# Performance work log

Measured on AMD Instinct MI355X. Metric: run time of the kernel, lower is better.

The kernel has to match this reference:

```python
import jax, jax.numpy as jnp
import numpy as np

NEG_SLOPE = 0.2   # PyG GATConv default negative_slope
BN_EPS = 1e-5


def gat_layer(x, src, dst, W, a_src, a_dst, b, num_nodes):
    """PyG-style GATConv (concat=True). src/dst already include self-loops."""
    H, C = a_src.shape
    h = (x @ W).reshape(num_nodes, H, C)            # [N,H,C]
    al_s = jnp.sum(h * a_src, axis=-1)              # [N,H] per-node src score
    al_d = jnp.sum(h * a_dst, axis=-1)              # [N,H]
    e = al_s[src] + al_d[dst]                       # [E,H]
    e = jnp.where(e > 0, e, NEG_SLOPE * e)          # leaky_relu
    m = jax.ops.segment_max(e, dst, num_segments=num_nodes)
    e = jnp.exp(e - m[dst])
    s = jax.ops.segment_sum(e, dst, num_segments=num_nodes)
    alpha = e / (s[dst] + 1e-16)                    # segment softmax over dst
    out = jax.ops.segment_sum(alpha[:, :, None] * h[src], dst, num_segments=num_nodes)
    return out.reshape(num_nodes, H * C) + b


def batch_norm(x, gamma, beta):
    mu = jnp.mean(x, axis=0)
    var = jnp.mean((x - mu) ** 2, axis=0)
    return (x - mu) * jax.lax.rsqrt(var + BN_EPS) * gamma + beta


def setup_inputs() -> dict:
    N, E, IN, H, C, L, OUT, NC = 50000, 800000, 256, 4, 64, 32, 32, 30
    HC = H * C
    key = jax.random.key(0)
    cnt = [0]
    def nk():
        cnt[0] += 1
        return jax.random.fold_in(key, cnt[0])
    def w(shape, scale):
        return jax.random.normal(nk(), shape, jnp.float32) * scale
    inp = {
        "x": jax.random.normal(nk(), (N, IN), jnp.float32),
        "edge_index": jax.random.randint(nk(), (2, E), 0, N, dtype=jnp.int32),
        "eps": jax.random.normal(nk(), (N, L), jnp.float32),
    }
    for i, d_in in zip((1, 2, 3), (IN, HC, HC)):
        inp[f"W{i}"] = w((d_in, HC), 1.0 / np.sqrt(d_in))
        inp[f"asrc{i}"] = w((H, C), 0.1)
        inp[f"adst{i}"] = w((H, C), 0.1)
        inp[f"b{i}"] = jnp.zeros((HC,), jnp.float32)
        inp[f"g{i}"] = jnp.ones((HC,), jnp.float32)
        inp[f"be{i}"] = jnp.zeros((HC,), jnp.float32)
    inp["Wr"] = w((IN, HC), 1.0 / np.sqrt(IN)); inp["br"] = jnp.zeros((HC,), jnp.float32)
    inp["Wmu"] = w((HC, L), 1.0 / np.sqrt(HC)); inp["bmu"] = jnp.zeros((L,), jnp.float32)
    inp["Wlv"] = w((HC, L), 1.0 / np.sqrt(HC)); inp["blv"] = jnp.zeros((L,), jnp.float32)
    inp["Wd"] = w((L, OUT), 1.0 / np.sqrt(L)); inp["bd"] = jnp.zeros((OUT,), jnp.float32)
    inp["Wa"] = w((HC, NC), 1.0 / np.sqrt(HC)); inp["ba"] = jnp.zeros((NC,), jnp.float32)
    return inp


def reference(x, edge_index, eps,
              W1, asrc1, adst1, b1, g1, be1,
              W2, asrc2, adst2, b2, g2, be2,
              W3, asrc3, adst3, b3, g3, be3,
              Wr, br, Wmu, bmu, Wlv, blv, Wd, bd, Wa, ba):
    N = x.shape[0]
    loop = jnp.arange(N, dtype=edge_index.dtype)   # PyG add_self_loops default
    src = jnp.concatenate([edge_index[0], loop])
    dst = jnp.concatenate([edge_index[1], loop])

    residual = x @ Wr + br                          # [N, HC]
    h = jax.nn.relu(batch_norm(gat_layer(x, src, dst, W1, asrc1, adst1, b1, N), g1, be1))
    h = jax.nn.relu(batch_norm(gat_layer(h, src, dst, W2, asrc2, adst2, b2, N), g2, be2))
    h = jax.nn.relu(batch_norm(gat_layer(h, src, dst, W3, asrc3, adst3, b3, N), g3, be3))
    enc = h + residual

    mu = enc @ Wmu + bmu
    logvar = enc @ Wlv + blv
    z = mu + eps * jnp.exp(0.5 * logvar)            # reparameterize
    out = z @ Wd + bd
    aux_out = enc @ Wa + ba
    return (out, mu, logvar, aux_out, enc)
```

## Files before the change

### kernel.cpp

```cpp
#include <hip/hip_runtime.h>
#include <cstdint>

typedef __bf16 bf16;
typedef float f32x4 __attribute__((ext_vector_type(4)));
typedef _Float16 fp16;
typedef _Float16 half8 __attribute__((ext_vector_type(8)));

#define NEG_SLOPE 0.2f
#define BN_EPS 1e-5f

__device__ __forceinline__ void gld_lds16(const void* g, void* l) {
  auto gp = reinterpret_cast<const __attribute__((address_space(1))) unsigned int*>(
      reinterpret_cast<uintptr_t>(g));
  auto lp = reinterpret_cast<__attribute__((address_space(3))) unsigned int*>(
      reinterpret_cast<uintptr_t>(l));
  __builtin_amdgcn_global_load_lds(gp, lp, 16, 0, 0);
}

__global__ void k_init_counts(int* counts, int N) {
  int i = blockIdx.x * 256 + threadIdx.x;
  if (i < N) counts[i] = 1;
}

__global__ void k_count(const int* __restrict__ ei, int* counts, int E) {
  int i = blockIdx.x * 256 + threadIdx.x;
  if (i < E) atomicAdd(&counts[ei[E + i]], 1);
}

__global__ __launch_bounds__(256) void k_scan1(const int* __restrict__ counts,
                                               int* __restrict__ row_start,
                                               int* __restrict__ bsums, int N) {
  __shared__ int s[256];
  const int t = threadIdx.x;
  const int idx = blockIdx.x * 1024 + t * 4;
  int a0 = (idx + 0 < N) ? counts[idx + 0] : 0;
  int a1 = (idx + 1 < N) ? counts[idx + 1] : 0;
  int a2 = (idx + 2 < N) ? counts[idx + 2] : 0;
  int a3 = (idx + 3 < N) ? counts[idx + 3] : 0;
  const int mysum = a0 + a1 + a2 + a3;
  s[t] = mysum;
  __syncthreads();
  for (int ofs = 1; ofs < 256; ofs <<= 1) {
    int v = (t >= ofs) ? s[t - ofs] : 0;
    __syncthreads();
    s[t] += v;
    __syncthreads();
  }
  int excl = s[t] - mysum;
  if (idx + 0 < N) row_start[idx + 0] = excl;
  if (idx + 1 < N) row_start[idx + 1] = excl + a0;
  if (idx + 2 < N) row_start[idx + 2] = excl + a0 + a1;
  if (idx + 3 < N) row_start[idx + 3] = excl + a0 + a1 + a2;
  if (t == 255) bsums[blockIdx.x] = s[255];
}

__global__ void k_scan2(int* __restrict__ bsums, int* __restrict__ row_start, int nb, int N) {
  if (threadIdx.x == 0 && blockIdx.x == 0) {
    int run = 0;
    for (int i = 0; i < nb; ++i) {
      int v = bsums[i];
      bsums[i] = run;
      run += v;
    }
    row_start[N] = run;
  }
}

__global__ void k_scan3(int* __restrict__ row_start, int* __restrict__ cursor,
                        const int* __restrict__ bsums, int N) {
  int i = blockIdx.x * 256 + threadIdx.x;
  if (i < N) {
    int v = row_start[i] + bsums[i >> 10];
    row_start[i] = v;
    cursor[i] = v;
  }
}

__global__ void k_fill(const int* __restrict__ ei, int* cursor, int* __restrict__ csr_src,
                       int E, int N) {
  int i = blockIdx.x * 256 + threadIdx.x;
  if (i < E) {
    int s = ei[i], d = ei[E + i];
    int p = atomicAdd(&cursor[d], 1);
    csr_src[p] = s;
  } else if (i < E + N) {
    int n = i - E;
    int p = atomicAdd(&cursor[n], 1);
    csr_src[p] = n;
  }
}

__global__ void k_tofp16(const float* __restrict__ src, fp16* __restrict__ dst, int n) {
  int i = blockIdx.x * 256 + threadIdx.x;
  if (i < n) dst[i] = (fp16)src[i];
}

__global__ void k_transpose_w(const float* __restrict__ W, fp16* __restrict__ Wt) {
  int k = blockIdx.x, n = threadIdx.x;
  Wt[n * 256 + k] = (fp16)W[k * 256 + n];
}

__global__ void k_build_head_w(const float* __restrict__ Wmu, const float* __restrict__ bmu,
                               const float* __restrict__ Wlv, const float* __restrict__ blv,
                               const float* __restrict__ Wa, const float* __restrict__ ba,
                               fp16* __restrict__ Wh, float* __restrict__ bias_cat) {
  int k = blockIdx.x, n = threadIdx.x;
  float v = 0.f;
  if (n < 32) v = Wmu[k * 32 + n];
  else if (n < 64) v = Wlv[k * 32 + (n - 32)];
  else if (n < 94) v = Wa[k * 30 + (n - 64)];
  Wh[n * 256 + k] = (fp16)v;
  if (k == 0) {
    float b = 0.f;
    if (n < 32) b = bmu[n];
    else if (n < 64) b = blv[n - 32];
    else if (n < 94) b = ba[n - 64];
    bias_cat[n] = b;
  }
}

__global__ __launch_bounds__(256) void k_gemm(
    const fp16* __restrict__ A16, const fp16* __restrict__ B16,
    const float* __restrict__ bias, float* __restrict__ Cf, fp16* __restrict__ C16,
    const float* __restrict__ asrcp, const float* __restrict__ adstp,
    float* __restrict__ alsp, float* __restrict__ aldp,
    int M, int ldc) {
  __shared__ fp16 Ash[128 * 32];
  __shared__ fp16 Bsh[128 * 32];
  const int t = threadIdx.x;
  const int wave = t >> 6, lane = t & 63;
  const int m0 = blockIdx.x * 128, n0 = blockIdx.y * 128;
  const int lrow = lane & 15, lq = lane >> 4;
  const int wm = (wave >> 1) * 64, wn = (wave & 1) * 64;

  f32x4 acc[4][4] = {};

  const int j0 = wave * 64 + lane, j1 = j0 + 256;
  const int ar0 = j0 >> 2, ar1 = j1 >> 2;
  const int ak0 = ((j0 & 3) ^ ((ar0 >> 1) & 3)) * 8;
  const int ak1 = ((j1 & 3) ^ ((ar1 >> 1) & 3)) * 8;
  const int gm0 = min(m0 + ar0, M - 1), gm1 = min(m0 + ar1, M - 1);
  const size_t oa0 = (size_t)gm0 * 256 + ak0, oa1 = (size_t)gm1 * 256 + ak1;
  const size_t ob0 = (size_t)(n0 + ar0) * 256 + ak0, ob1 = (size_t)(n0 + ar1) * 256 + ak1;
  const int l0 = wave * 512, l1 = 2048 + wave * 512;

  for (int k0 = 0; k0 < 256; k0 += 32) {
    __syncthreads();
    gld_lds16(A16 + oa0 + k0, Ash + l0);
    gld_lds16(A16 + oa1 + k0, Ash + l1);
    gld_lds16(B16 + ob0 + k0, Bsh + l0);
    gld_lds16(B16 + ob1 + k0, Bsh + l1);
    __syncthreads();
    half8 af[4], bf[4];
#pragma unroll
    for (int mi = 0; mi < 4; mi++) {
      int row = wm + mi * 16 + lrow;
      int off = row * 32 + ((lq ^ ((row >> 1) & 3)) << 3);
      af[mi] = *(const half8*)(Ash + off);
    }
#pragma unroll
    for (int ni = 0; ni < 4; ni++) {
      int row = wn + ni * 16 + lrow;
      int off = row * 32 + ((lq ^ ((row >> 1) & 3)) << 3);
      bf[ni] = *(const half8*)(Bsh + off);
    }
#pragma unroll
    for (int mi = 0; mi < 4; mi++)
#pragma unroll
      for (int ni = 0; ni < 4; ni++)
        acc[mi][ni] = __builtin_amdgcn_mfma_f32_16x16x32_f16(af[mi], bf[ni], acc[mi][ni], 0, 0, 0);
  }

#pragma unroll
  for (int mi = 0; mi < 4; mi++) {
    const int mb = m0 + wm + mi * 16 + lq * 4;
#pragma unroll
    for (int ni = 0; ni < 4; ni++) {
      const int n = n0 + wn + ni * 16 + lrow;
#pragma unroll
      for (int r = 0; r < 4; r++) {
        int m = mb + r;
        if (m < M) {
          if (C16) C16[(size_t)m * ldc + n] = (fp16)acc[mi][ni][r];
          else     Cf[(size_t)m * ldc + n] = acc[mi][ni][r] + (bias ? bias[n] : 0.f);
        }
      }
    }
  }

  if (asrcp) {
    const int headg = (n0 + wn) >> 6;
    float as4[4], ad4[4];
#pragma unroll
    for (int ni = 0; ni < 4; ni++) {
      int cg = n0 + wn + ni * 16 + lrow;
      as4[ni] = asrcp[cg];
      ad4[ni] = adstp[cg];
    }
#pragma unroll
    for (int mi = 0; mi < 4; mi++) {
      float ps[4] = {0.f, 0.f, 0.f, 0.f}, pd[4] = {0.f, 0.f, 0.f, 0.f};
#pragma unroll
      for (int ni = 0; ni < 4; ni++)
#pragma unroll
        for (int r = 0; r < 4; r++) {
          ps[r] += acc[mi][ni][r] * as4[ni];
          pd[r] += acc[mi][ni][r] * ad4[ni];
        }
#pragma unroll
      for (int o = 1; o < 16; o <<= 1)
#pragma unroll
        for (int r = 0; r < 4; r++) {
          ps[r] += __shfl_xor(ps[r], o, 64);
          pd[r] += __shfl_xor(pd[r], o, 64);
        }
      if (lrow == 0) {
#pragma unroll
        for (int r = 0; r < 4; r++) {
          int m = m0 + wm + mi * 16 + lq * 4 + r;
          if (m < M) {
            alsp[(size_t)m * 4 + headg] = ps[r];
            aldp[(size_t)m * 4 + headg] = pd[r];
          }
        }
      }
    }
  }
}

__global__ __launch_bounds__(256) void k_gather(
    const fp16* __restrict__ h16, const float* __restrict__ als, const float* __restrict__ ald,
    const int* __restrict__ row_start, const int* __restrict__ csr_src,
    const float* __restrict__ bias, fp16* __restrict__ out, float* __restrict__ stats, int N) {
  if (blockIdx.x == 0) { stats[threadIdx.x] = 0.f; stats[256 + threadIdx.x] = 0.f; }
  const int wave = threadIdx.x >> 6, lane = threadIdx.x & 63;
  const int half = lane >> 5, l32 = lane & 31;
  const int n = blockIdx.x * 8 + wave * 2 + half;
  if (n >= N) return;
  const int head = l32 >> 3;
  const int c0 = l32 * 8;
  const float adh = ald[(size_t)n * 4 + head];
  const int beg = row_start[n], end = row_start[n + 1];
  float s = 0.f;
  float acc[8] = {0.f, 0.f, 0.f, 0.f, 0.f, 0.f, 0.f, 0.f};
#pragma unroll 4
  for (int i = beg; i < end; ++i) {
    const int sidx = csr_src[i];
    float e = als[(size_t)sidx * 4 + head] + adh;
    e = e > 0.f ? e : NEG_SLOPE * e;
    const float w = __expf(e);
    s += w;
    const half8 hv = *(const half8*)(h16 + (size_t)sidx * 256 + c0);
#pragma unroll
    for (int k = 0; k < 8; ++k) acc[k] += w * (float)hv[k];
  }
  const float inv = 1.f / (s + 1e-16f);
  const float4 b1 = *(const float4*)(bias + c0);
  const float4 b2 = *(const float4*)(bias + c0 + 4);
  half8 o;
  o[0] = (fp16)(acc[0] * inv + b1.x); o[1] = (fp16)(acc[1] * inv + b1.y);
  o[2] = (fp16)(acc[2] * inv + b1.z); o[3] = (fp16)(acc[3] * inv + b1.w);
  o[4] = (fp16)(acc[4] * inv + b2.x); o[5] = (fp16)(acc[5] * inv + b2.y);
  o[6] = (fp16)(acc[6] * inv + b2.z); o[7] = (fp16)(acc[7] * inv + b2.w);
  *(half8*)(out + (size_t)n * 256 + c0) = o;
}

__global__ __launch_bounds__(256) void k_bn_stats(const fp16* __restrict__ x,
                                                  float* __restrict__ stats, int N) {
  const int t = threadIdx.x;
  int r0 = blockIdx.x * 128;
  int rend = min(r0 + 128, N);
  float s = 0.f, sq = 0.f;
  for (int r = r0; r < rend; ++r) {
    float v = (float)x[(size_t)r * 256 + t];
    s += v; sq += v * v;
  }
  atomicAdd(&stats[t], s);
  atomicAdd(&stats[256 + t], sq);
}

__global__ __launch_bounds__(256) void k_bn_apply(
    const fp16* __restrict__ x, const float* __restrict__ stats,
    const float* __restrict__ g, const float* __restrict__ be,
    fp16* __restrict__ act16, float* __restrict__ encf,
    float invN, int total) {
  int idx = blockIdx.x * 256 + threadIdx.x;
  if (idx >= total) return;
  int c = idx & 255;
  float mu = stats[c] * invN;
  float var = stats[256 + c] * invN - mu * mu;
  float v = ((float)x[idx] - mu) * rsqrtf(var + BN_EPS) * g[c] + be[c];
  v = fmaxf(v, 0.f);
  if (encf) { v += encf[idx]; encf[idx] = v; }
  act16[idx] = (fp16)v;
}

__global__ __launch_bounds__(256) void k_finish(
    const float* __restrict__ HEAD, const float* __restrict__ eps,
    const float* __restrict__ Wd, const float* __restrict__ bd,
    float* __restrict__ o_out, float* __restrict__ o_mu, float* __restrict__ o_lv,
    float* __restrict__ o_aux, int N) {
  __shared__ float sWd[1024];
  __shared__ float sZ[8][33];
  const int t = threadIdx.x;
  for (int i = t; i < 1024; i += 256) sWd[i] = Wd[i];
  __syncthreads();
  const int r = t >> 5, j = t & 31;
  const int n = blockIdx.x * 8 + r;
  if (n < N) {
    const float* hp = HEAD + (size_t)n * 128;
    float mu = hp[j];
    float lv = hp[32 + j];
    float z = mu + eps[(size_t)n * 32 + j] * __expf(0.5f * lv);
    sZ[r][j] = z;
    o_mu[(size_t)n * 32 + j] = mu;
    o_lv[(size_t)n * 32 + j] = lv;
    if (j < 30) o_aux[(size_t)n * 30 + j] = hp[64 + j];
  }
  __syncthreads();
  if (n < N) {
    float o = bd[j];
#pragma unroll
    for (int k = 0; k < 32; ++k) o += sZ[r][k] * sWd[k * 32 + j];
    o_out[(size_t)n * 32 + j] = o;
  }
}

extern "C" void kernel_launch(void* const* d_in, const int* in_sizes, int n_in,
                              void* d_out, int out_size, void* d_ws, size_t ws_size,
                              hipStream_t stream) {
  const float* x   = (const float*)d_in[0];
  const int*   ei  = (const int*)d_in[1];
  const float* eps = (const float*)d_in[2];
  const float* Wg[3]   = {(const float*)d_in[3], (const float*)d_in[9],  (const float*)d_in[15]};
  const float* asrc[3] = {(const float*)d_in[4], (const float*)d_in[10], (const float*)d_in[16]};
  const float* adst[3] = {(const float*)d_in[5], (const float*)d_in[11], (const float*)d_in[17]};
  const float* bg[3]   = {(const float*)d_in[6], (const float*)d_in[12], (const float*)d_in[18]};
  const float* gam[3]  = {(const float*)d_in[7], (const float*)d_in[13], (const float*)d_in[19]};
  const float* bet[3]  = {(const float*)d_in[8], (const float*)d_in[14], (const float*)d_in[20]};
  const float* Wr  = (const float*)d_in[21];
  const float* br  = (const float*)d_in[22];
  const float* Wmu = (const float*)d_in[23];
  const float* bmu = (const float*)d_in[24];
  const float* Wlv = (const float*)d_in[25];
  const float* blv = (const float*)d_in[26];
  const float* Wd  = (const float*)d_in[27];
  const float* bd  = (const float*)d_in[28];
  const float* Wa  = (const float*)d_in[29];
  const float* ba  = (const float*)d_in[30];

  const int N = in_sizes[0] / 256;
  const int E = in_sizes[1] / 2;

  float* outp  = (float*)d_out;
  float* o_out = outp;
  float* o_mu  = outp + (size_t)N * 32;
  float* o_lv  = outp + (size_t)N * 64;
  float* o_aux = outp + (size_t)N * 96;
  float* o_enc = outp + (size_t)N * 96 + (size_t)N * 30;

  char* p = (char*)d_ws;
  auto carve = [&](size_t bytes) -> char* {
    char* r = p;
    p += (bytes + 255) & ~(size_t)255;
    return r;
  };
  int* counts    = (int*)carve((size_t)N * 4);
  int* row_start = (int*)carve(((size_t)N + 1) * 4);
  int* cursor    = (int*)carve((size_t)N * 4);
  int* csr_src   = (int*)carve((size_t)(E + N) * 4);
  int* bsums     = (int*)carve(((size_t)N / 1024 + 2) * 4);
  fp16* Wt16[4];
  for (int i = 0; i < 4; ++i) Wt16[i] = (fp16*)carve(256 * 256 * 2);
  fp16* Wh16 = (fp16*)carve(128 * 256 * 2);
  float* bias_cat = (float*)carve(128 * 4);
  fp16* A16 = (fp16*)carve((size_t)N * 256 * 2);
  fp16* H16 = (fp16*)carve((size_t)N * 256 * 2);
  float* FHEAD = (float*)carve((size_t)N * 128 * 4);
  fp16* AGG16 = (fp16*)carve((size_t)N * 256 * 2);
  float* als = (float*)carve((size_t)N * 4 * 4);
  float* ald = (float*)carve((size_t)N * 4 * 4);
  float* stats = (float*)carve(512 * 4);

  dim3 b256(256);

  const int nb_scan = (N + 1023) / 1024;
  k_init_counts<<<(N + 255) / 256, b256, 0, stream>>>(counts, N);
  k_count<<<(E + 255) / 256, b256, 0, stream>>>(ei, counts, E);
  k_scan1<<<nb_scan, b256, 0, stream>>>(counts, row_start, bsums, N);
  k_scan2<<<1, 64, 0, stream>>>(bsums, row_start, nb_scan, N);
  k_scan3<<<(N + 255) / 256, b256, 0, stream>>>(row_start, cursor, bsums, N);
  k_fill<<<(E + N + 255) / 256, b256, 0, stream>>>(ei, cursor, csr_src, E, N);

  k_tofp16<<<((size_t)N * 256 + 255) / 256, b256, 0, stream>>>(x, A16, N * 256);
  k_transpose_w<<<256, b256, 0, stream>>>(Wr, Wt16[0]);
  for (int l = 0; l < 3; ++l)
    k_transpose_w<<<256, b256, 0, stream>>>(Wg[l], Wt16[l + 1]);
  k_build_head_w<<<256, dim3(128), 0, stream>>>(Wmu, bmu, Wlv, blv, Wa, ba, Wh16, bias_cat);

  dim3 ggrid((N + 127) / 128, 2);
  k_gemm<<<ggrid, b256, 0, stream>>>(A16, Wt16[0], br, o_enc, nullptr,
                                     nullptr, nullptr, nullptr, nullptr, N, 256);

  const float invN = 1.0f / (float)N;
  for (int l = 0; l < 3; ++l) {
    k_gemm<<<ggrid, b256, 0, stream>>>(A16, Wt16[l + 1], nullptr, nullptr, H16,
                                       asrc[l], adst[l], als, ald, N, 256);
    k_gather<<<(N + 7) / 8, b256, 0, stream>>>(H16, als, ald, row_start, csr_src, bg[l],
                                               AGG16, stats, N);
    k_bn_stats<<<(N + 127) / 128, b256, 0, stream>>>(AGG16, stats, N);
    if (l < 2)
      k_bn_apply<<<((size_t)N * 256 + 255) / 256, b256, 0, stream>>>(
          AGG16, stats, gam[l], bet[l], A16, nullptr, invN, N * 256);
    else
      k_bn_apply<<<((size_t)N * 256 + 255) / 256, b256, 0, stream>>>(
          AGG16, stats, gam[l], bet[l], A16, o_enc, invN, N * 256);
  }

  dim3 hgrid((N + 127) / 128, 1);
  k_gemm<<<hgrid, b256, 0, stream>>>(A16, Wh16, bias_cat, FHEAD, nullptr,
                                     nullptr, nullptr, nullptr, nullptr, N, 128);
  k_finish<<<(N + 7) / 8, b256, 0, stream>>>(FHEAD, eps, Wd, bd, o_out, o_mu, o_lv, o_aux, N);
}
```

Measured before the change: 812.2 us.

## Split gather feature columns across XCD halves for L2 locality

```diff
diff --git a/kernel.cpp b/kernel.cpp
--- a/kernel.cpp
+++ b/kernel.cpp
@@ -5,6 +5,7 @@
 typedef float f32x4 __attribute__((ext_vector_type(4)));
 typedef _Float16 fp16;
 typedef _Float16 half8 __attribute__((ext_vector_type(8)));
+typedef _Float16 half4 __attribute__((ext_vector_type(4)));
 
 #define NEG_SLOPE 0.2f
 #define BN_EPS 1e-5f
@@ -231,18 +232,24 @@
 __global__ __launch_bounds__(256) void k_gather(
     const fp16* __restrict__ h16, const float* __restrict__ als, const float* __restrict__ ald,
     const int* __restrict__ row_start, const int* __restrict__ csr_src,
-    const float* __restrict__ bias, fp16* __restrict__ out, float* __restrict__ stats, int N) {
+    const float* __restrict__ bias, fp16* __restrict__ out, float* __restrict__ stats,
+    int N, int nb) {
   if (blockIdx.x == 0) { stats[threadIdx.x] = 0.f; stats[256 + threadIdx.x] = 0.f; }
+  const int b = blockIdx.x;
+  const int xcd = b & 7;
+  const int hc = xcd >> 2;
+  const int g = (b >> 3) * 4 + (xcd & 3);
+  if (g >= nb) return;
   const int wave = threadIdx.x >> 6, lane = threadIdx.x & 63;
   const int half = lane >> 5, l32 = lane & 31;
-  const int n = blockIdx.x * 8 + wave * 2 + half;
+  const int n = g * 8 + wave * 2 + half;
   if (n >= N) return;
-  const int head = l32 >> 3;
-  const int c0 = l32 * 8;
+  const int c = hc * 128 + l32 * 4;
+  const int head = c >> 6;
   const float adh = ald[(size_t)n * 4 + head];
   const int beg = row_start[n], end = row_start[n + 1];
   float s = 0.f;
-  float acc[8] = {0.f, 0.f, 0.f, 0.f, 0.f, 0.f, 0.f, 0.f};
+  float a0 = 0.f, a1 = 0.f, a2 = 0.f, a3 = 0.f;
 #pragma unroll 4
   for (int i = beg; i < end; ++i) {
     const int sidx = csr_src[i];
@@ -250,19 +257,16 @@
     e = e > 0.f ? e : NEG_SLOPE * e;
     const float w = __expf(e);
     s += w;
-    const half8 hv = *(const half8*)(h16 + (size_t)sidx * 256 + c0);
-#pragma unroll
-    for (int k = 0; k < 8; ++k) acc[k] += w * (float)hv[k];
+    const half4 hv = *(const half4*)(h16 + (size_t)sidx * 256 + c);
+    a0 += w * (float)hv[0]; a1 += w * (float)hv[1];
+    a2 += w * (float)hv[2]; a3 += w * (float)hv[3];
   }
   const float inv = 1.f / (s + 1e-16f);
-  const float4 b1 = *(const float4*)(bias + c0);
-  const float4 b2 = *(const float4*)(bias + c0 + 4);
-  half8 o;
-  o[0] = (fp16)(acc[0] * inv + b1.x); o[1] = (fp16)(acc[1] * inv + b1.y);
-  o[2] = (fp16)(acc[2] * inv + b1.z); o[3] = (fp16)(acc[3] * inv + b1.w);
-  o[4] = (fp16)(acc[4] * inv + b2.x); o[5] = (fp16)(acc[5] * inv + b2.y);
-  o[6] = (fp16)(acc[6] * inv + b2.z); o[7] = (fp16)(acc[7] * inv + b2.w);
-  *(half8*)(out + (size_t)n * 256 + c0) = o;
+  const float4 bb = *(const float4*)(bias + c);
+  half4 o;
+  o[0] = (fp16)(a0 * inv + bb.x); o[1] = (fp16)(a1 * inv + bb.y);
+  o[2] = (fp16)(a2 * inv + bb.z); o[3] = (fp16)(a3 * inv + bb.w);
+  *(half4*)(out + (size_t)n * 256 + c) = o;
 }
 
 __global__ __launch_bounds__(256) void k_bn_stats(const fp16* __restrict__ x,
@@ -403,11 +407,13 @@
                                      nullptr, nullptr, nullptr, nullptr, N, 256);
 
   const float invN = 1.0f / (float)N;
+  const int nb_gather = (N + 7) / 8;
+  const int grid_gather = 8 * ((nb_gather + 3) / 4);
   for (int l = 0; l < 3; ++l) {
     k_gemm<<<ggrid, b256, 0, stream>>>(A16, Wt16[l + 1], nullptr, nullptr, H16,
                                        asrc[l], adst[l], als, ald, N, 256);
-    k_gather<<<(N + 7) / 8, b256, 0, stream>>>(H16, als, ald, row_start, csr_src, bg[l],
-                                               AGG16, stats, N);
+    k_gather<<<grid_gather, b256, 0, stream>>>(H16, als, ald, row_start, csr_src, bg[l],
+                                               AGG16, stats, N, nb_gather);
     k_bn_stats<<<(N + 127) / 128, b256, 0, stream>>>(AGG16, stats, N);
     if (l < 2)
       k_bn_apply<<<((size_t)N * 256 + 255) / 256, b256, 0, stream>>>(
```

Result: no change. 817.1 us (+0.6%).
